# Kernel tuning notes

Measured on AMD Instinct MI355X. Metric: run time of the kernel, lower is better.

The kernel has to match this reference:

```python
import jax, jax.numpy as jnp
import numpy as np

B, N, M, R, W, H, NIN, OUT = 32, 1024, 64, 4, 1, 512, 256, 256
RM = 1 + 2 * W  # read modes: backward(W), content(1), forward(W)
SIZES = [W*M, W*M, R, W, W, R*RM, W*M, W, R*M, R]
OFFS = np.cumsum([0] + SIZES)
P = int(OFFS[-1])
EPS = 1e-8


def setup_inputs():
    key = jax.random.key(0)
    ks = jax.random.split(key, 20)
    norm = lambda w: w / jnp.sum(w, axis=-1, keepdims=True)
    return {
        'X': jax.random.normal(ks[0], (B, NIN), jnp.float32),
        'backward_embeddings': jax.random.normal(ks[1], (B, H), jnp.float32),
        'memory': jax.random.normal(ks[2], (B, N, M), jnp.float32) * 0.1,
        'prev_read': jax.random.normal(ks[3], (B, R, M), jnp.float32) * 0.01,
        'h0': jax.random.normal(ks[4], (B, H), jnp.float32) * 0.1,
        'c0': jax.random.normal(ks[5], (B, H), jnp.float32) * 0.1,
        'read_w_prev': norm(jax.random.uniform(ks[6], (B, R, N), jnp.float32)),
        'write_w_prev': norm(jax.random.uniform(ks[7], (B, W, N), jnp.float32)),
        'usage_prev': jax.random.uniform(ks[8], (B, W, N), jnp.float32) * 0.5,
        'prec_prev': norm(jax.random.uniform(ks[9], (B, W, N), jnp.float32)),
        'links_prev': jnp.zeros((B, W, N, N), jnp.float32),
        'lstm_Wx': jax.random.normal(ks[10], (NIN + R * M, 4 * H), jnp.float32) * 0.02,
        'lstm_Wh': jax.random.normal(ks[11], (H, 4 * H), jnp.float32) * 0.02,
        'lstm_b': jnp.zeros((4 * H,), jnp.float32),
        'para_W': jax.random.normal(ks[12], (2 * H, P), jnp.float32) * 0.02,
        'para_b': jax.random.normal(ks[13], (P,), jnp.float32) * 0.01,
        'ln_g': jnp.ones((P,), jnp.float32),
        'ln_b': jnp.zeros((P,), jnp.float32),
        'proc_W': jax.random.normal(ks[14], (2 * H + R * M, OUT), jnp.float32) * 0.02,
        'proc_b': jnp.zeros((OUT,), jnp.float32),
    }


def _content(keys, beta, mem):
    # cosine-similarity content addressing: keys [B,h,M], beta [B,h], mem [B,N,M] -> [B,h,N]
    kn = keys / (jnp.linalg.norm(keys, axis=-1, keepdims=True) + EPS)
    mn = mem / (jnp.linalg.norm(mem, axis=-1, keepdims=True) + EPS)
    sim = jnp.einsum('bhm,bnm->bhn', kn, mn)
    return jax.nn.softmax(beta[..., None] * sim, axis=-1)


def _layernorm(x, g, b):
    mu = jnp.mean(x, axis=-1, keepdims=True)
    var = jnp.var(x, axis=-1, keepdims=True)
    return (x - mu) / jnp.sqrt(var + 1e-5) * g + b


def reference(X, backward_embeddings, memory, prev_read, h0, c0,
              read_w_prev, write_w_prev, usage_prev, prec_prev, links_prev,
              lstm_Wx, lstm_Wh, lstm_b, para_W, para_b, ln_g, ln_b, proc_W, proc_b):
    # ---- controller (single LSTM step) ----
    inp = jnp.concatenate([X, prev_read.reshape(B, R * M)], axis=1)
    gates = inp @ lstm_Wx + h0 @ lstm_Wh + lstm_b
    i, f, g, o = jnp.split(gates, 4, axis=1)
    c = jax.nn.sigmoid(f) * c0 + jax.nn.sigmoid(i) * jnp.tanh(g)
    h = jax.nn.sigmoid(o) * jnp.tanh(c)  # c_output [B,H]

    # ---- param_operations ----
    pvec = _layernorm(jnp.concatenate([h, backward_embeddings], axis=1) @ para_W + para_b, ln_g, ln_b)
    sl = lambda k: pvec[:, OFFS[k]:OFFS[k + 1]]
    write_vectors = sl(0).reshape(B, W, M)
    erase_vectors = jax.nn.sigmoid(sl(1)).reshape(B, W, M)
    free_gate = jax.nn.sigmoid(sl(2))                      # [B,R]
    alloc_gate = jax.nn.sigmoid(sl(3))                     # [B,W]
    write_gate = jax.nn.sigmoid(sl(4))                     # [B,W]
    read_mode = jax.nn.softmax(sl(5).reshape(B, R, RM), axis=2)
    write_keys = sl(6).reshape(B, W, M)
    write_strengths = 1.0 + jax.nn.softplus(sl(7))         # [B,W]
    read_keys = sl(8).reshape(B, R, M)
    read_strengths = 1.0 + jax.nn.softplus(sl(9))          # [B,R]

    # ---- usage + allocation ----
    psi = jnp.prod(1.0 - free_gate[:, :, None] * read_w_prev, axis=1)          # [B,N]
    usage = (usage_prev + write_w_prev - usage_prev * write_w_prev) * psi[:, None, :]  # [B,W,N]
    order = jnp.argsort(usage, axis=-1)
    u_sorted = jnp.take_along_axis(usage, order, axis=-1)
    vals = (1.0 - u_sorted) * jnp.cumprod(u_sorted, axis=-1)  # inclusive cumprod (as in source)
    inv = jnp.argsort(order, axis=-1)
    alloc = jnp.take_along_axis(vals, inv, axis=-1)           # [B,W,N]

    # ---- write weights ----
    wc = _content(write_keys, write_strengths, memory)        # [B,W,N]
    ww = write_gate[..., None] * (alloc_gate[..., None] * alloc + (1.0 - alloc_gate[..., None]) * wc)

    # ---- memory write (sequential over write heads) ----
    mem = memory
    for wi in range(W):
        w = ww[:, wi]                                         # [B,N]
        mem = mem * (1.0 - w[:, :, None] * erase_vectors[:, wi, None, :]) \
              + w[:, :, None] * write_vectors[:, wi, None, :]

    # ---- temporal links ----
    eye = jnp.eye(N, dtype=mem.dtype)
    new_links, new_prec = [], []
    for wi in range(W):
        w = ww[:, wi]
        p = prec_prev[:, wi]
        L = links_prev[:, wi]
        Lnew = (1.0 - w[:, :, None] - w[:, None, :]) * L + w[:, :, None] * p[:, None, :]
        Lnew = Lnew * (1.0 - eye)                             # zero diagonal
        new_links.append(Lnew)
        new_prec.append((1.0 - jnp.sum(w, axis=1, keepdims=True)) * p + w)
    links = jnp.stack(new_links, axis=1)                      # [B,W,N,N]

    # ---- read weights: backward(W) | content | forward(W) ----
    rc = _content(read_keys, read_strengths, mem)             # [B,R,N]
    fwd = jnp.einsum('bwij,brj->bwri', links, read_w_prev)    # L @ w_prev
    bwd = jnp.einsum('bwji,brj->bwri', links, read_w_prev)    # L^T @ w_prev
    rw = read_mode[:, :, W][..., None] * rc
    for wi in range(W):
        rw = rw + read_mode[:, :, wi][..., None] * bwd[:, wi] \
                + read_mode[:, :, W + 1 + wi][..., None] * fwd[:, wi]

    # ---- reads + output projection ----
    reads = jnp.einsum('brn,bnm->brm', rw, mem)               # [B,R,M]
    out = jnp.concatenate([h, backward_embeddings, reads.reshape(B, R * M)], axis=1) @ proc_W + proc_b
    return out
```

## Files before the change

kernel.cpp:

```cpp
#include <hip/hip_runtime.h>
#include <math.h>

#define Bb 32
#define Nn 1024
#define Mm 64
#define Rr 4
#define Hh 512
#define NINq 256
#define Pp 471
#define EPSN 1e-8f

__device__ __forceinline__ float sigm(float x){ return 1.0f/(1.0f+expf(-x)); }

__global__ __launch_bounds__(256) void k_gates(
    const float* __restrict__ X, const float* __restrict__ pr,
    const float* __restrict__ h0, const float* __restrict__ Wx,
    const float* __restrict__ Wh, float* __restrict__ gpart)
{
  __shared__ float lin[32][64];
  int tid = threadIdx.x;
  int col = blockIdx.x*64 + (tid & 63);
  int bg  = tid >> 6;
  int k0  = blockIdx.y*64;
#pragma unroll
  for (int q=0;q<8;q++){
    int idx = tid + 256*q;
    int bb = idx >> 6, kk = idx & 63;
    int k = k0 + kk;
    float v;
    if (k < 256)      v = X [bb*NINq + k];
    else if (k < 512) v = pr[bb*(Rr*Mm) + (k-256)];
    else              v = h0[bb*Hh + (k-512)];
    lin[bb][kk] = v;
  }
  __syncthreads();
  const float* Wr = (k0 < 512) ? (Wx + (size_t)k0*2048)
                               : (Wh + (size_t)(k0-512)*2048);
  float acc[8];
#pragma unroll
  for (int i=0;i<8;i++) acc[i]=0.f;
#pragma unroll 8
  for (int kk=0; kk<64; ++kk){
    float wv = Wr[(size_t)kk*2048 + col];
#pragma unroll
    for (int bb=0; bb<8; ++bb) acc[bb] += wv * lin[bg*8+bb][kk];
  }
  float* gp = gpart + (size_t)blockIdx.y*65536;
#pragma unroll
  for (int bb=0; bb<8; ++bb)
    gp[(bg*8+bb)*2048 + col] = acc[bb];
}

__global__ void k_lstm_ep(const float* __restrict__ gpart, const float* __restrict__ lb,
                          const float* __restrict__ c0, const float* __restrict__ emb,
                          float* __restrict__ hcat, float* __restrict__ ocat)
{
  int idx = blockIdx.x*blockDim.x + threadIdx.x;
  if (idx >= Bb*Hh) return;
  int b = idx >> 9, j = idx & 511;
  float gi = lb[j], gf = lb[j+512], gg = lb[j+1024], go = lb[j+1536];
  for (int c=0;c<16;++c){
    const float* gp = gpart + (size_t)c*65536 + b*2048;
    gi += gp[j]; gf += gp[j+512]; gg += gp[j+1024]; go += gp[j+1536];
  }
  float c = sigm(gf)*c0[idx] + sigm(gi)*tanhf(gg);
  float h = sigm(go)*tanhf(c);
  float e = emb[idx];
  hcat[b*1024 + j]       = h;
  hcat[b*1024 + 512 + j] = e;
  ocat[b*1280 + j]       = h;
  ocat[b*1280 + 512 + j] = e;
  if (j < 256) ocat[b*1280 + 1024 + j] = 0.f;
}

__global__ __launch_bounds__(256) void k_para(
    const float* __restrict__ hcat, const float* __restrict__ Wp,
    float* __restrict__ ppart)
{
  __shared__ float lin[32][64];
  int tid = threadIdx.x;
  int col = blockIdx.x*64 + (tid & 63);
  int bg  = tid >> 6;
  int k0  = blockIdx.y*64;
#pragma unroll
  for (int q=0;q<8;q++){
    int idx = tid + 256*q;
    int bb = idx >> 6, kk = idx & 63;
    lin[bb][kk] = hcat[bb*1024 + k0 + kk];
  }
  __syncthreads();
  int colc = (col < Pp) ? col : (Pp-1);
  const float* Wr = Wp + (size_t)k0*Pp;
  float acc[8];
#pragma unroll
  for (int i=0;i<8;i++) acc[i]=0.f;
#pragma unroll 8
  for (int kk=0; kk<64; ++kk){
    float wv = Wr[(size_t)kk*Pp + colc];
#pragma unroll
    for (int bb=0; bb<8; ++bb) acc[bb] += wv * lin[bg*8+bb][kk];
  }
  if (col < Pp) {
    float* pp = ppart + (size_t)blockIdx.y*16384;
#pragma unroll
    for (int bb=0; bb<8; ++bb)
      pp[(bg*8+bb)*512 + col] = acc[bb];
  }
}

__global__ __launch_bounds__(1024) void k_lnalloc(
    const float* __restrict__ ppart, const float* __restrict__ bp,
    const float* __restrict__ ln_g, const float* __restrict__ ln_b,
    const float* __restrict__ rwp, const float* __restrict__ wwp,
    const float* __restrict__ up,
    float* __restrict__ pvec, float* __restrict__ alloc)
{
  __shared__ float red[8];
  __shared__ float fg[4];
  __shared__ unsigned long long sk[1024];
  __shared__ float wsums[16];
  int b = blockIdx.x, tid = threadIdx.x;
  int lane = tid & 63, wv = tid >> 6;
  float acc = 0.f, d = 0.f;
  if (tid < 512) {
    if (tid < Pp) {
      acc = bp[tid];
#pragma unroll
      for (int c=0;c<16;++c) acc += ppart[(size_t)c*16384 + b*512 + tid];
    }
    float s = acc;
    for (int o=32;o;o>>=1) s += __shfl_xor(s,o,64);
    if (lane==0) red[wv] = s;
  }
  __syncthreads();
  if (tid < 8){ float xx = red[tid]; for (int o=4;o;o>>=1) xx += __shfl_xor(xx,o,64); if (!tid) red[0]=xx; }
  __syncthreads();
  float mu = red[0] / (float)Pp;
  __syncthreads();
  if (tid < 512) {
    d = (tid < Pp) ? (acc - mu) : 0.f;
    float s2 = d*d;
    for (int o=32;o;o>>=1) s2 += __shfl_xor(s2,o,64);
    if (lane==0) red[wv] = s2;
  }
  __syncthreads();
  if (tid < 8){ float xx = red[tid]; for (int o=4;o;o>>=1) xx += __shfl_xor(xx,o,64); if (!tid) red[0]=xx; }
  __syncthreads();
  float var = red[0] / (float)Pp;
  if (tid < Pp) {
    float y = d / sqrtf(var + 1e-5f) * ln_g[tid] + ln_b[tid];
    pvec[b*512 + tid] = y;
    if (tid >= 128 && tid < 132) fg[tid-128] = sigm(y);
  }
  __syncthreads();
  float psi = 1.f;
#pragma unroll
  for (int r=0;r<4;r++) psi *= 1.f - fg[r]*rwp[b*(Rr*Nn) + r*Nn + tid];
  float u = up[b*Nn+tid], w = wwp[b*Nn+tid];
  float usage = (u + w - u*w)*psi;
  unsigned long long key = ((unsigned long long)__float_as_uint(usage) << 32) | (unsigned)tid;
  for (int k=2; k<=1024; k<<=1) {
    for (int j=k>>1; j>0; j>>=1) {
      bool lower = (tid & j) == 0;
      bool asc   = (tid & k) == 0;
      unsigned long long pk;
      if (j >= 64) {
        sk[tid] = key; __syncthreads();
        pk = sk[tid ^ j];
        __syncthreads();
      } else {
        pk = __shfl_xor(key, j, 64);
      }
      key = ((key < pk) == (lower == asc)) ? key : pk;
    }
  }
  float us = __uint_as_float((unsigned)(key >> 32));
  int order = (int)(key & 1023u);
  float v = us;
#pragma unroll
  for (int dd=1; dd<64; dd<<=1) {
    float p = __shfl_up(v, dd, 64);
    if (lane >= dd) v *= p;
  }
  if (lane == 63) wsums[wv] = v;
  __syncthreads();
  if (wv == 0) {
    float t = (lane < 16) ? wsums[lane] : 1.f;
#pragma unroll
    for (int dd=1; dd<16; dd<<=1) {
      float p = __shfl_up(t, dd, 64);
      if (lane >= dd) t *= p;
    }
    if (lane < 16) wsums[lane] = t;
  }
  __syncthreads();
  float prefix = (wv > 0) ? wsums[wv-1] : 1.f;
  alloc[b*Nn + order] = (1.f - us) * (v * prefix);
}

__global__ __launch_bounds__(256) void k_simw(
    const float* __restrict__ pvec, const float* __restrict__ mem,
    float* __restrict__ simw)
{
  __shared__ float kdir[64];
  __shared__ float sc[1];
  int b = blockIdx.y, tid = threadIdx.x;
  int wv = tid>>6, lane = tid&63;
  const float* pv = pvec + b*512;
  if (wv == 0) {
    float v = pv[146 + lane];
    float s = v*v;
    for (int o=32;o;o>>=1) s += __shfl_xor(s,o,64);
    kdir[lane] = v / (sqrtf(s) + EPSN);
    if (lane == 0) sc[0] = 1.f + log1pf(expf(pv[210]));
  }
  __syncthreads();
  float beta = sc[0];
  for (int t=0;t<16;++t){
    int n = blockIdx.x*64 + wv*16 + t;
    float v = mem[(b*Nn+n)*Mm + lane];
    float d = v*kdir[lane], s2 = v*v;
    for (int o=32;o;o>>=1){ d += __shfl_xor(d,o,64); s2 += __shfl_xor(s2,o,64); }
    if (lane == 0) simw[b*Nn+n] = beta * d / (sqrtf(s2) + EPSN);
  }
}

__global__ __launch_bounds__(1024) void k_ww2(
    const float* __restrict__ pvec, const float* __restrict__ simw,
    const float* __restrict__ alloc, const float* __restrict__ prec,
    const float* __restrict__ rwp, float* __restrict__ wwb, float* __restrict__ spsw)
{
  __shared__ float red[16];
  __shared__ float red8[16][8];
  __shared__ float scal[2];
  int b = blockIdx.x, tid = threadIdx.x;
  int wv = tid >> 6, lane = tid & 63;
  const float* pv = pvec + b*512;
  if (tid == 0) { scal[0] = sigm(pv[132]); scal[1] = sigm(pv[133]); }
  float v = simw[b*Nn + tid];
  float m_ = v;
  for (int o=32;o;o>>=1) m_ = fmaxf(m_, __shfl_xor(m_,o,64));
  if (lane==0) red[wv] = m_;
  __syncthreads();
  if (tid < 16){ float x = red[tid]; for (int o=8;o;o>>=1) x = fmaxf(x,__shfl_xor(x,o,64)); if (!tid) red[0]=x; }
  __syncthreads();
  float gmax = red[0];
  __syncthreads();
  float e = expf(v - gmax);
  float ss = e;
  for (int o=32;o;o>>=1) ss += __shfl_xor(ss,o,64);
  if (lane==0) red[wv] = ss;
  __syncthreads();
  if (tid < 16){ float x = red[tid]; for (int o=8;o;o>>=1) x += __shfl_xor(x,o,64); if (!tid) red[0]=x; }
  __syncthreads();
  float wcn = e / red[0];
  float ag = scal[0], wg = scal[1];
  float an = alloc[b*Nn + tid];
  float wwn = wg * (ag*an + (1.f-ag)*wcn);
  wwb[b*Nn + tid] = wwn;
  float p = prec[b*Nn + tid];
#pragma unroll
  for (int r=0;r<4;r++){
    float a = rwp[b*(Rr*Nn) + r*Nn + tid];
    float x1 = p*a, x2 = wwn*a;
    for (int o=32;o;o>>=1){ x1 += __shfl_xor(x1,o,64); x2 += __shfl_xor(x2,o,64); }
    if (lane==0){ red8[wv][r] = x1; red8[wv][4+r] = x2; }
  }
  __syncthreads();
  if (tid < 8) {
    float s = 0.f;
    for (int w2=0; w2<16; ++w2) s += red8[w2][tid];
    spsw[b*8 + tid] = s;
  }
}

__global__ __launch_bounds__(256) void k_memupd(
    const float* __restrict__ pvec, const float* __restrict__ mem,
    const float* __restrict__ wwb, float* __restrict__ memn, float* __restrict__ simr)
{
  __shared__ float ev[64], wvv[64];
  __shared__ float kdir[4][64];
  __shared__ float beta[4];
  int b = blockIdx.y, tid = threadIdx.x;
  int wv = tid>>6, lane = tid&63;
  const float* pv = pvec + b*512;
  {
    float kv = pv[211 + wv*64 + lane];
    float s = kv*kv;
    for (int o=32;o;o>>=1) s += __shfl_xor(s,o,64);
    kdir[wv][lane] = kv/(sqrtf(s)+EPSN);
    if (lane==0) beta[wv] = 1.f + log1pf(expf(pv[467+wv]));
  }
  if (tid < 64) { wvv[tid] = pv[tid]; ev[tid] = sigm(pv[64+tid]); }
  __syncthreads();
  for (int t=0;t<16;++t){
    int n = blockIdx.x*64 + wv*16 + t;
    float wwn = wwb[b*Nn + n];
    float v = mem[(b*Nn+n)*Mm + lane];
    float nv = v*(1.f - wwn*ev[lane]) + wwn*wvv[lane];
    memn[(b*Nn+n)*Mm + lane] = nv;
    float s2 = nv*nv;
    float d0 = nv*kdir[0][lane], d1 = nv*kdir[1][lane];
    float d2 = nv*kdir[2][lane], d3 = nv*kdir[3][lane];
    for (int o=32;o;o>>=1){
      s2 += __shfl_xor(s2,o,64);
      d0 += __shfl_xor(d0,o,64); d1 += __shfl_xor(d1,o,64);
      d2 += __shfl_xor(d2,o,64); d3 += __shfl_xor(d3,o,64);
    }
    if (lane==0){
      float inv = 1.f/(sqrtf(s2)+EPSN);
      simr[(b*4+0)*Nn+n] = beta[0]*d0*inv;
      simr[(b*4+1)*Nn+n] = beta[1]*d1*inv;
      simr[(b*4+2)*Nn+n] = beta[2]*d2*inv;
      simr[(b*4+3)*Nn+n] = beta[3]*d3*inv;
    }
  }
}

__global__ __launch_bounds__(256) void k_links(
    const float* __restrict__ links, const float* __restrict__ rwp,
    const float* __restrict__ wwb,
    float* __restrict__ S1p, float* __restrict__ S2p,
    float* __restrict__ T1p, float* __restrict__ T2p,
    float* __restrict__ diag)
{
  __shared__ float tile[64][65];
  __shared__ float ai[4][64], wai[4][64], aj[4][64], waj[4][64];
  int b = blockIdx.y;
  int stripe = blockIdx.x >> 1, half = blockIdx.x & 1;
  int i0 = stripe*64, jbase = half*512;
  int tid = threadIdx.x;
  {
    int r = tid>>6, ii = tid&63;
    float a = rwp[b*(Rr*Nn) + r*Nn + i0+ii];
    ai[r][ii]  = a;
    wai[r][ii] = a * wwb[b*Nn + i0+ii];
  }
  float s1a[4]={0,0,0,0}, s2a[4]={0,0,0,0};
  const float* Lb = links + (size_t)b*Nn*Nn;
  const int lrow = tid>>4, c4 = tid&15;
  float4 pv[4];
#pragma unroll
  for (int q=0;q<4;q++)
    pv[q] = *reinterpret_cast<const float4*>(&Lb[(size_t)(i0+lrow+16*q)*Nn + jbase + c4*4]);
  const int dt = (half == (stripe>>3)) ? (stripe&7) : -1;
  for (int t=0; t<8; ++t) {
    int j0 = jbase + t*64;
    __syncthreads();
#pragma unroll
    for (int q=0;q<4;q++){
      int row = lrow + 16*q;
      float4 v = pv[q];
      tile[row][c4*4+0]=v.x; tile[row][c4*4+1]=v.y;
      tile[row][c4*4+2]=v.z; tile[row][c4*4+3]=v.w;
    }
    {
      int r = tid>>6, jj = tid&63;
      float a = rwp[b*(Rr*Nn) + r*Nn + j0+jj];
      aj[r][jj]  = a;
      waj[r][jj] = a * wwb[b*Nn + j0+jj];
    }
    __syncthreads();
    if (t < 7) {
      int j0n = j0 + 64;
#pragma unroll
      for (int q=0;q<4;q++)
        pv[q] = *reinterpret_cast<const float4*>(&Lb[(size_t)(i0+lrow+16*q)*Nn + j0n + c4*4]);
    }
    if (t == dt && tid < 64) diag[b*Nn + i0 + tid] = tile[tid][tid];
    {
      int ii = tid>>2, c = tid&3;
      float p1[4]={0,0,0,0}, p2[4]={0,0,0,0};
      for (int k=0;k<16;k++){
        int jj = c*16+k;
        float v = tile[ii][jj];
#pragma unroll
        for (int r=0;r<4;r++){ p1[r] += v*aj[r][jj]; p2[r] += v*waj[r][jj]; }
      }
#pragma unroll
      for (int r=0;r<4;r++){
        p1[r] += __shfl_xor(p1[r],1,64); p1[r] += __shfl_xor(p1[r],2,64);
        p2[r] += __shfl_xor(p2[r],1,64); p2[r] += __shfl_xor(p2[r],2,64);
      }
      if (c==0){
#pragma unroll
        for (int r=0;r<4;r++){ s1a[r] += p1[r]; s2a[r] += p2[r]; }
      }
    }
    {
      int jj = tid>>2, q = tid&3;
      float p1[4]={0,0,0,0}, p2[4]={0,0,0,0};
      for (int k=0;k<16;k++){
        int ii = q*16+k;
        float v = tile[ii][jj];
#pragma unroll
        for (int r=0;r<4;r++){ p1[r] += v*ai[r][ii]; p2[r] += v*wai[r][ii]; }
      }
#pragma unroll
      for (int r=0;r<4;r++){
        p1[r] += __shfl_xor(p1[r],1,64); p1[r] += __shfl_xor(p1[r],2,64);
        p2[r] += __shfl_xor(p2[r],1,64); p2[r] += __shfl_xor(p2[r],2,64);
      }
      if (q==0){
#pragma unroll
        for (int r=0;r<4;r++){
          size_t o = (size_t)(((b*4+r)*16 + stripe))*Nn + j0 + jj;
          T1p[o] = p1[r];
          T2p[o] = p2[r];
        }
      }
    }
  }
  if ((tid&3)==0){
    int ii = tid>>2;
#pragma unroll
    for (int r=0;r<4;r++){
      size_t o = (size_t)(((half*Bb + b)*4 + r))*Nn + i0 + ii;
      S1p[o] = s1a[r];
      S2p[o] = s2a[r];
    }
  }
}

__global__ __launch_bounds__(1024) void k_rsoft(
    const float* __restrict__ pvec, const float* __restrict__ rwp,
    const float* __restrict__ prec, const float* __restrict__ wwb,
    const float* __restrict__ T1p, const float* __restrict__ T2p,
    const float* __restrict__ S1p, const float* __restrict__ S2p,
    const float* __restrict__ spsw, const float* __restrict__ diag,
    float* __restrict__ simr)
{
  __shared__ float red[16];
  __shared__ float rm3[3];
  int b = blockIdx.x, r = blockIdx.y, tid = threadIdx.x;
  int wv = tid>>6, lane = tid&63;
  const float* pv = pvec + b*512;
  if (tid == 0) {
    float x0 = pv[134+r*3], x1 = pv[134+r*3+1], x2 = pv[134+r*3+2];
    float mx = fmaxf(x0, fmaxf(x1,x2));
    float e0 = expf(x0-mx), e1 = expf(x1-mx), e2 = expf(x2-mx);
    float s = e0+e1+e2;
    rm3[0]=e0/s; rm3[1]=e1/s; rm3[2]=e2/s;
  }
  float v = simr[(b*4+r)*Nn + tid];
  float m_ = v;
  for (int o=32;o;o>>=1) m_ = fmaxf(m_, __shfl_xor(m_,o,64));
  if (lane==0) red[wv]=m_;
  __syncthreads();
  if (tid<16){ float x=red[tid]; for(int o=8;o;o>>=1) x=fmaxf(x,__shfl_xor(x,o,64)); if(!tid) red[0]=x; }
  __syncthreads();
  float gmax = red[0];
  __syncthreads();
  float e = expf(v-gmax);
  float s = e;
  for (int o=32;o;o>>=1) s += __shfl_xor(s,o,64);
  if (lane==0) red[wv]=s;
  __syncthreads();
  if (tid<16){ float x=red[tid]; for(int o=8;o;o>>=1) x+=__shfl_xor(x,o,64); if(!tid) red[0]=x; }
  __syncthreads();
  float rc = e/red[0];
  float s1v = S1p[(size_t)((0*Bb+b)*4+r)*Nn + tid] + S1p[(size_t)((1*Bb+b)*4+r)*Nn + tid];
  float s2v = S2p[(size_t)((0*Bb+b)*4+r)*Nn + tid] + S2p[(size_t)((1*Bb+b)*4+r)*Nn + tid];
  float t1v = 0.f, t2v = 0.f;
#pragma unroll
  for (int st=0; st<16; ++st){
    size_t o = (size_t)((b*4+r)*16 + st)*Nn + tid;
    t1v += T1p[o];
    t2v += T2p[o];
  }
  float w_n = wwb[b*Nn + tid];
  float p_n = prec[b*Nn + tid];
  float a = rwp[b*(Rr*Nn)+r*Nn+tid];
  float Lii = diag[b*Nn + tid];
  float Spr = spsw[b*8+r], Swr = spsw[b*8+4+r];
  float fwd = (1.f-w_n)*(s1v - Lii*a) - (s2v - Lii*w_n*a) + w_n*(Spr - p_n*a);
  float bwd = (1.f-w_n)*(t1v - Lii*a) - (t2v - w_n*Lii*a) + p_n*(Swr - w_n*a);
  simr[(b*4+r)*Nn + tid] = rm3[1]*rc + rm3[0]*bwd + rm3[2]*fwd;
}

__global__ __launch_bounds__(256) void k_rgemv(
    const float* __restrict__ simr, const float* __restrict__ memn,
    const float* __restrict__ bo, float* __restrict__ ocat, float* __restrict__ out)
{
  int b = blockIdx.y, ch = blockIdx.x, tid = threadIdx.x;
  if (ch == 0) out[b*256 + tid] = bo[tid];
  int r = tid>>6, m = tid&63;
  float acc = 0.f;
#pragma unroll 8
  for (int t=0;t<64;++t){
    int n = ch*64 + t;
    acc += simr[(b*4+r)*Nn + n] * memn[(b*Nn+n)*Mm + m];
  }
  atomicAdd(&ocat[b*1280 + 1024 + r*64 + m], acc);
}

__global__ __launch_bounds__(256) void k_gout(
    const float* __restrict__ ocat, const float* __restrict__ Wo,
    float* __restrict__ out)
{
  __shared__ float lin[32][64];
  int tid = threadIdx.x;
  int col = blockIdx.x*64 + (tid & 63);
  int bg  = tid >> 6;
  int k0  = blockIdx.y*64;
#pragma unroll
  for (int q=0;q<8;q++){
    int idx = tid + 256*q;
    int bb = idx >> 6, kk = idx & 63;
    lin[bb][kk] = ocat[bb*1280 + k0 + kk];
  }
  __syncthreads();
  const float* Wr = Wo + (size_t)k0*256;
  float acc[8];
#pragma unroll
  for (int i=0;i<8;i++) acc[i]=0.f;
#pragma unroll 8
  for (int kk=0; kk<64; ++kk){
    float wv = Wr[(size_t)kk*256 + col];
#pragma unroll
    for (int bb=0; bb<8; ++bb) acc[bb] += wv * lin[bg*8+bb][kk];
  }
#pragma unroll
  for (int bb=0; bb<8; ++bb)
    atomicAdd(&out[(size_t)(bg*8+bb)*256 + col], acc[bb]);
}

extern "C" void kernel_launch(void* const* d_in, const int* in_sizes, int n_in,
                              void* d_out, int out_size, void* d_ws, size_t ws_size,
                              hipStream_t stream)
{
  (void)in_sizes; (void)n_in; (void)out_size; (void)ws_size;
  const float* X    = (const float*)d_in[0];
  const float* emb  = (const float*)d_in[1];
  const float* mem  = (const float*)d_in[2];
  const float* prvr = (const float*)d_in[3];
  const float* h0   = (const float*)d_in[4];
  const float* c0   = (const float*)d_in[5];
  const float* rwp  = (const float*)d_in[6];
  const float* wwp  = (const float*)d_in[7];
  const float* up   = (const float*)d_in[8];
  const float* prec = (const float*)d_in[9];
  const float* links= (const float*)d_in[10];
  const float* Wx   = (const float*)d_in[11];
  const float* Wh   = (const float*)d_in[12];
  const float* lb   = (const float*)d_in[13];
  const float* Wp   = (const float*)d_in[14];
  const float* bp   = (const float*)d_in[15];
  const float* lng  = (const float*)d_in[16];
  const float* lnb  = (const float*)d_in[17];
  const float* Wo   = (const float*)d_in[18];
  const float* bo   = (const float*)d_in[19];
  float* out = (float*)d_out;
  float* ws  = (float*)d_ws;

  float* memn  = ws;
  float* T1p   = memn  + 2097152;
  float* T2p   = T1p   + 2097152;
  float* S1p   = T2p   + 2097152;
  float* S2p   = S1p   + 262144;
  float* gpart = S2p   + 262144;
  float* ppart = gpart + 1048576;
  float* pvec  = ppart + 262144;
  float* alloc = pvec  + 16384;
  float* wwb   = alloc + 32768;
  float* ocat  = wwb   + 32768;
  float* spsw  = ocat  + 40960;
  float* simr  = spsw  + 256;
  float* diag  = simr  + 131072;
  float* hcat  = diag  + 32768;

  k_gates  <<<dim3(32,16),  dim3(256),  0, stream>>>(X, prvr, h0, Wx, Wh, gpart);
  k_lstm_ep<<<dim3(64),     dim3(256),  0, stream>>>(gpart, lb, c0, emb, hcat, ocat);
  k_para   <<<dim3(8,16),   dim3(256),  0, stream>>>(hcat, Wp, ppart);
  k_lnalloc<<<dim3(32),     dim3(1024), 0, stream>>>(ppart, bp, lng, lnb, rwp, wwp, up, pvec, alloc);
  k_simw   <<<dim3(16,32),  dim3(256),  0, stream>>>(pvec, mem, simr);
  k_ww2    <<<dim3(32),     dim3(1024), 0, stream>>>(pvec, simr, alloc, prec, rwp, wwb, spsw);
  k_memupd <<<dim3(16,32),  dim3(256),  0, stream>>>(pvec, mem, wwb, memn, simr);
  k_links  <<<dim3(32,32),  dim3(256),  0, stream>>>(links, rwp, wwb, S1p, S2p, T1p, T2p, diag);
  k_rsoft  <<<dim3(32,4),   dim3(1024), 0, stream>>>(pvec, rwp, prec, wwb, T1p, T2p, S1p, S2p, spsw, diag, simr);
  k_rgemv  <<<dim3(16,32),  dim3(256),  0, stream>>>(simr, memn, bo, ocat, out);
  k_gout   <<<dim3(4,20),   dim3(256),  0, stream>>>(ocat, Wo, out);
}
```

Baseline: 134.9 us.

## Fuse write-addressing, links/memory update, and read path into fewer kernels

Folds the write-content similarity and the write-weight softmax into the layernorm/allocation kernel, so the allocation vector stays in shared memory. The memory update and read-content similarity now run as extra blocks of the links kernel, and the read softmax, read weighting and read GEMV are merged into one per-batch kernel that no longer needs atomics. Eleven launches become seven and several global round trips go away. In exchange, the write-similarity and read-GEMV work now runs on only 32 blocks, each doing per-thread row loads, so parallelism on those parts drops.

```diff
diff --git a/kernel.cpp b/kernel.cpp
--- a/kernel.cpp
+++ b/kernel.cpp
@@ -70,7 +70,6 @@
   hcat[b*1024 + 512 + j] = e;
   ocat[b*1280 + j]       = h;
   ocat[b*1280 + 512 + j] = e;
-  if (j < 256) ocat[b*1280 + 1024 + j] = 0.f;
 }
 
 __global__ __launch_bounds__(256) void k_para(
@@ -108,17 +107,23 @@
   }
 }
 
-__global__ __launch_bounds__(1024) void k_lnalloc(
+__global__ __launch_bounds__(1024) void k_waddr(
     const float* __restrict__ ppart, const float* __restrict__ bp,
     const float* __restrict__ ln_g, const float* __restrict__ ln_b,
     const float* __restrict__ rwp, const float* __restrict__ wwp,
-    const float* __restrict__ up,
-    float* __restrict__ pvec, float* __restrict__ alloc)
-{
-  __shared__ float red[8];
+    const float* __restrict__ up, const float* __restrict__ mem,
+    const float* __restrict__ prec,
+    float* __restrict__ pvec, float* __restrict__ wwb, float* __restrict__ spsw)
+{
+  __shared__ float red[16];
+  __shared__ float pvs[512];
   __shared__ float fg[4];
+  __shared__ float kdir[64];
+  __shared__ float scal[4];
   __shared__ unsigned long long sk[1024];
   __shared__ float wsums[16];
+  __shared__ float af[1024];
+  __shared__ float red8[16][8];
   int b = blockIdx.x, tid = threadIdx.x;
   int lane = tid & 63, wv = tid >> 6;
   float acc = 0.f, d = 0.f;
@@ -150,7 +155,20 @@
   if (tid < Pp) {
     float y = d / sqrtf(var + 1e-5f) * ln_g[tid] + ln_b[tid];
     pvec[b*512 + tid] = y;
-    if (tid >= 128 && tid < 132) fg[tid-128] = sigm(y);
+    pvs[tid] = y;
+  }
+  __syncthreads();
+  if (tid < 4) fg[tid] = sigm(pvs[128+tid]);
+  if (wv == 0) {
+    float v = pvs[146 + lane];
+    float s = v*v;
+    for (int o=32;o;o>>=1) s += __shfl_xor(s,o,64);
+    kdir[lane] = v / (sqrtf(s) + EPSN);
+  }
+  if (tid == 0) {
+    scal[0] = sigm(pvs[132]);
+    scal[1] = sigm(pvs[133]);
+    scal[2] = 1.f + log1pf(expf(pvs[210]));
   }
   __syncthreads();
   float psi = 1.f;
@@ -195,50 +213,18 @@
   }
   __syncthreads();
   float prefix = (wv > 0) ? wsums[wv-1] : 1.f;
-  alloc[b*Nn + order] = (1.f - us) * (v * prefix);
-}
-
-__global__ __launch_bounds__(256) void k_simw(
-    const float* __restrict__ pvec, const float* __restrict__ mem,
-    float* __restrict__ simw)
-{
-  __shared__ float kdir[64];
-  __shared__ float sc[1];
-  int b = blockIdx.y, tid = threadIdx.x;
-  int wv = tid>>6, lane = tid&63;
-  const float* pv = pvec + b*512;
-  if (wv == 0) {
-    float v = pv[146 + lane];
-    float s = v*v;
-    for (int o=32;o;o>>=1) s += __shfl_xor(s,o,64);
-    kdir[lane] = v / (sqrtf(s) + EPSN);
-    if (lane == 0) sc[0] = 1.f + log1pf(expf(pv[210]));
-  }
-  __syncthreads();
-  float beta = sc[0];
-  for (int t=0;t<16;++t){
-    int n = blockIdx.x*64 + wv*16 + t;
-    float v = mem[(b*Nn+n)*Mm + lane];
-    float d = v*kdir[lane], s2 = v*v;
-    for (int o=32;o;o>>=1){ d += __shfl_xor(d,o,64); s2 += __shfl_xor(s2,o,64); }
-    if (lane == 0) simw[b*Nn+n] = beta * d / (sqrtf(s2) + EPSN);
-  }
-}
-
-__global__ __launch_bounds__(1024) void k_ww2(
-    const float* __restrict__ pvec, const float* __restrict__ simw,
-    const float* __restrict__ alloc, const float* __restrict__ prec,
-    const float* __restrict__ rwp, float* __restrict__ wwb, float* __restrict__ spsw)
-{
-  __shared__ float red[16];
-  __shared__ float red8[16][8];
-  __shared__ float scal[2];
-  int b = blockIdx.x, tid = threadIdx.x;
-  int wv = tid >> 6, lane = tid & 63;
-  const float* pv = pvec + b*512;
-  if (tid == 0) { scal[0] = sigm(pv[132]); scal[1] = sigm(pv[133]); }
-  float v = simw[b*Nn + tid];
-  float m_ = v;
+  af[order] = (1.f - us) * (v * prefix);
+  float beta = scal[2];
+  float dot = 0.f, s2 = 0.f;
+  const float* mrow = mem + (size_t)(b*Nn + tid)*Mm;
+#pragma unroll
+  for (int j=0;j<16;j++){
+    float4 mv = *reinterpret_cast<const float4*>(&mrow[j*4]);
+    dot += mv.x*kdir[j*4] + mv.y*kdir[j*4+1] + mv.z*kdir[j*4+2] + mv.w*kdir[j*4+3];
+    s2  += mv.x*mv.x + mv.y*mv.y + mv.z*mv.z + mv.w*mv.w;
+  }
+  float sim = beta * dot / (sqrtf(s2) + EPSN);
+  float m_ = sim;
   for (int o=32;o;o>>=1) m_ = fmaxf(m_, __shfl_xor(m_,o,64));
   if (lane==0) red[wv] = m_;
   __syncthreads();
@@ -246,7 +232,7 @@
   __syncthreads();
   float gmax = red[0];
   __syncthreads();
-  float e = expf(v - gmax);
+  float e = expf(sim - gmax);
   float ss = e;
   for (int o=32;o;o>>=1) ss += __shfl_xor(ss,o,64);
   if (lane==0) red[wv] = ss;
@@ -255,8 +241,7 @@
   __syncthreads();
   float wcn = e / red[0];
   float ag = scal[0], wg = scal[1];
-  float an = alloc[b*Nn + tid];
-  float wwn = wg * (ag*an + (1.f-ag)*wcn);
+  float wwn = wg * (ag*af[tid] + (1.f-ag)*wcn);
   wwb[b*Nn + tid] = wwn;
   float p = prec[b*Nn + tid];
 #pragma unroll
@@ -274,62 +259,60 @@
   }
 }
 
-__global__ __launch_bounds__(256) void k_memupd(
-    const float* __restrict__ pvec, const float* __restrict__ mem,
-    const float* __restrict__ wwb, float* __restrict__ memn, float* __restrict__ simr)
-{
-  __shared__ float ev[64], wvv[64];
-  __shared__ float kdir[4][64];
-  __shared__ float beta[4];
-  int b = blockIdx.y, tid = threadIdx.x;
-  int wv = tid>>6, lane = tid&63;
-  const float* pv = pvec + b*512;
-  {
-    float kv = pv[211 + wv*64 + lane];
-    float s = kv*kv;
-    for (int o=32;o;o>>=1) s += __shfl_xor(s,o,64);
-    kdir[wv][lane] = kv/(sqrtf(s)+EPSN);
-    if (lane==0) beta[wv] = 1.f + log1pf(expf(pv[467+wv]));
-  }
-  if (tid < 64) { wvv[tid] = pv[tid]; ev[tid] = sigm(pv[64+tid]); }
-  __syncthreads();
-  for (int t=0;t<16;++t){
-    int n = blockIdx.x*64 + wv*16 + t;
-    float wwn = wwb[b*Nn + n];
-    float v = mem[(b*Nn+n)*Mm + lane];
-    float nv = v*(1.f - wwn*ev[lane]) + wwn*wvv[lane];
-    memn[(b*Nn+n)*Mm + lane] = nv;
-    float s2 = nv*nv;
-    float d0 = nv*kdir[0][lane], d1 = nv*kdir[1][lane];
-    float d2 = nv*kdir[2][lane], d3 = nv*kdir[3][lane];
-    for (int o=32;o;o>>=1){
-      s2 += __shfl_xor(s2,o,64);
-      d0 += __shfl_xor(d0,o,64); d1 += __shfl_xor(d1,o,64);
-      d2 += __shfl_xor(d2,o,64); d3 += __shfl_xor(d3,o,64);
-    }
-    if (lane==0){
-      float inv = 1.f/(sqrtf(s2)+EPSN);
-      simr[(b*4+0)*Nn+n] = beta[0]*d0*inv;
-      simr[(b*4+1)*Nn+n] = beta[1]*d1*inv;
-      simr[(b*4+2)*Nn+n] = beta[2]*d2*inv;
-      simr[(b*4+3)*Nn+n] = beta[3]*d3*inv;
-    }
-  }
-}
-
-__global__ __launch_bounds__(256) void k_links(
+__global__ __launch_bounds__(256) void k_linksmem(
     const float* __restrict__ links, const float* __restrict__ rwp,
-    const float* __restrict__ wwb,
+    const float* __restrict__ wwb, const float* __restrict__ pvec,
+    const float* __restrict__ mem,
     float* __restrict__ S1p, float* __restrict__ S2p,
     float* __restrict__ T1p, float* __restrict__ T2p,
-    float* __restrict__ diag)
-{
+    float* __restrict__ diag, float* __restrict__ memn, float* __restrict__ simr)
+{
+  int b = blockIdx.y;
+  int tid = threadIdx.x;
+  if (blockIdx.x >= 32) {
+    __shared__ float ev[64], wvv[64];
+    __shared__ float kdir4[4][64];
+    __shared__ float beta4[4];
+    int stripe = blockIdx.x - 32;
+    int wv = tid>>6, lane = tid&63;
+    const float* pv = pvec + b*512;
+    {
+      float kv = pv[211 + wv*64 + lane];
+      float s = kv*kv;
+      for (int o=32;o;o>>=1) s += __shfl_xor(s,o,64);
+      kdir4[wv][lane] = kv/(sqrtf(s)+EPSN);
+      if (lane==0) beta4[wv] = 1.f + log1pf(expf(pv[467+wv]));
+    }
+    if (tid < 64) { wvv[tid] = pv[tid]; ev[tid] = sigm(pv[64+tid]); }
+    __syncthreads();
+    for (int t=0;t<16;++t){
+      int n = stripe*64 + wv*16 + t;
+      float wwn = wwb[b*Nn + n];
+      float v = mem[(b*Nn+n)*Mm + lane];
+      float nv = v*(1.f - wwn*ev[lane]) + wwn*wvv[lane];
+      memn[(b*Nn+n)*Mm + lane] = nv;
+      float s2 = nv*nv;
+      float d0 = nv*kdir4[0][lane], d1 = nv*kdir4[1][lane];
+      float d2 = nv*kdir4[2][lane], d3 = nv*kdir4[3][lane];
+      for (int o=32;o;o>>=1){
+        s2 += __shfl_xor(s2,o,64);
+        d0 += __shfl_xor(d0,o,64); d1 += __shfl_xor(d1,o,64);
+        d2 += __shfl_xor(d2,o,64); d3 += __shfl_xor(d3,o,64);
+      }
+      if (lane==0){
+        float inv = 1.f/(sqrtf(s2)+EPSN);
+        simr[(b*4+0)*Nn+n] = beta4[0]*d0*inv;
+        simr[(b*4+1)*Nn+n] = beta4[1]*d1*inv;
+        simr[(b*4+2)*Nn+n] = beta4[2]*d2*inv;
+        simr[(b*4+3)*Nn+n] = beta4[3]*d3*inv;
+      }
+    }
+    return;
+  }
   __shared__ float tile[64][65];
   __shared__ float ai[4][64], wai[4][64], aj[4][64], waj[4][64];
-  int b = blockIdx.y;
   int stripe = blockIdx.x >> 1, half = blockIdx.x & 1;
   int i0 = stripe*64, jbase = half*512;
-  int tid = threadIdx.x;
   {
     int r = tid>>6, ii = tid&63;
     float a = rwp[b*(Rr*Nn) + r*Nn + i0+ii];
@@ -422,76 +405,83 @@
   }
 }
 
-__global__ __launch_bounds__(1024) void k_rsoft(
+__global__ __launch_bounds__(1024) void k_rread(
     const float* __restrict__ pvec, const float* __restrict__ rwp,
     const float* __restrict__ prec, const float* __restrict__ wwb,
     const float* __restrict__ T1p, const float* __restrict__ T2p,
     const float* __restrict__ S1p, const float* __restrict__ S2p,
     const float* __restrict__ spsw, const float* __restrict__ diag,
-    float* __restrict__ simr)
-{
+    const float* __restrict__ simr, const float* __restrict__ memn,
+    const float* __restrict__ bo, float* __restrict__ ocat, float* __restrict__ out)
+{
+  __shared__ float rwl[4][1024];
   __shared__ float red[16];
-  __shared__ float rm3[3];
-  int b = blockIdx.x, r = blockIdx.y, tid = threadIdx.x;
+  __shared__ float rm3s[4][3];
+  __shared__ float rp[16][4][64];
+  int b = blockIdx.x, tid = threadIdx.x;
   int wv = tid>>6, lane = tid&63;
   const float* pv = pvec + b*512;
-  if (tid == 0) {
-    float x0 = pv[134+r*3], x1 = pv[134+r*3+1], x2 = pv[134+r*3+2];
+  if (tid < 4) {
+    float x0 = pv[134+tid*3], x1 = pv[134+tid*3+1], x2 = pv[134+tid*3+2];
     float mx = fmaxf(x0, fmaxf(x1,x2));
     float e0 = expf(x0-mx), e1 = expf(x1-mx), e2 = expf(x2-mx);
     float s = e0+e1+e2;
-    rm3[0]=e0/s; rm3[1]=e1/s; rm3[2]=e2/s;
-  }
-  float v = simr[(b*4+r)*Nn + tid];
-  float m_ = v;
-  for (int o=32;o;o>>=1) m_ = fmaxf(m_, __shfl_xor(m_,o,64));
-  if (lane==0) red[wv]=m_;
-  __syncthreads();
-  if (tid<16){ float x=red[tid]; for(int o=8;o;o>>=1) x=fmaxf(x,__shfl_xor(x,o,64)); if(!tid) red[0]=x; }
-  __syncthreads();
-  float gmax = red[0];
-  __syncthreads();
-  float e = expf(v-gmax);
-  float s = e;
-  for (int o=32;o;o>>=1) s += __shfl_xor(s,o,64);
-  if (lane==0) red[wv]=s;
-  __syncthreads();
-  if (tid<16){ float x=red[tid]; for(int o=8;o;o>>=1) x+=__shfl_xor(x,o,64); if(!tid) red[0]=x; }
-  __syncthreads();
-  float rc = e/red[0];
-  float s1v = S1p[(size_t)((0*Bb+b)*4+r)*Nn + tid] + S1p[(size_t)((1*Bb+b)*4+r)*Nn + tid];
-  float s2v = S2p[(size_t)((0*Bb+b)*4+r)*Nn + tid] + S2p[(size_t)((1*Bb+b)*4+r)*Nn + tid];
-  float t1v = 0.f, t2v = 0.f;
-#pragma unroll
-  for (int st=0; st<16; ++st){
-    size_t o = (size_t)((b*4+r)*16 + st)*Nn + tid;
-    t1v += T1p[o];
-    t2v += T2p[o];
+    rm3s[tid][0]=e0/s; rm3s[tid][1]=e1/s; rm3s[tid][2]=e2/s;
   }
   float w_n = wwb[b*Nn + tid];
   float p_n = prec[b*Nn + tid];
-  float a = rwp[b*(Rr*Nn)+r*Nn+tid];
   float Lii = diag[b*Nn + tid];
-  float Spr = spsw[b*8+r], Swr = spsw[b*8+4+r];
-  float fwd = (1.f-w_n)*(s1v - Lii*a) - (s2v - Lii*w_n*a) + w_n*(Spr - p_n*a);
-  float bwd = (1.f-w_n)*(t1v - Lii*a) - (t2v - w_n*Lii*a) + p_n*(Swr - w_n*a);
-  simr[(b*4+r)*Nn + tid] = rm3[1]*rc + rm3[0]*bwd + rm3[2]*fwd;
-}
-
-__global__ __launch_bounds__(256) void k_rgemv(
-    const float* __restrict__ simr, const float* __restrict__ memn,
-    const float* __restrict__ bo, float* __restrict__ ocat, float* __restrict__ out)
-{
-  int b = blockIdx.y, ch = blockIdx.x, tid = threadIdx.x;
-  if (ch == 0) out[b*256 + tid] = bo[tid];
-  int r = tid>>6, m = tid&63;
-  float acc = 0.f;
-#pragma unroll 8
+  __syncthreads();
+  for (int r=0;r<4;++r){
+    float v = simr[(b*4+r)*Nn + tid];
+    float m_ = v;
+    for (int o=32;o;o>>=1) m_ = fmaxf(m_, __shfl_xor(m_,o,64));
+    if (lane==0) red[wv]=m_;
+    __syncthreads();
+    if (tid<16){ float x=red[tid]; for(int o=8;o;o>>=1) x=fmaxf(x,__shfl_xor(x,o,64)); if(!tid) red[0]=x; }
+    __syncthreads();
+    float gmax = red[0];
+    __syncthreads();
+    float e = expf(v-gmax);
+    float s = e;
+    for (int o=32;o;o>>=1) s += __shfl_xor(s,o,64);
+    if (lane==0) red[wv]=s;
+    __syncthreads();
+    if (tid<16){ float x=red[tid]; for(int o=8;o;o>>=1) x+=__shfl_xor(x,o,64); if(!tid) red[0]=x; }
+    __syncthreads();
+    float rc = e/red[0];
+    float s1v = S1p[(size_t)((0*Bb+b)*4+r)*Nn + tid] + S1p[(size_t)((1*Bb+b)*4+r)*Nn + tid];
+    float s2v = S2p[(size_t)((0*Bb+b)*4+r)*Nn + tid] + S2p[(size_t)((1*Bb+b)*4+r)*Nn + tid];
+    float t1v = 0.f, t2v = 0.f;
+#pragma unroll
+    for (int st=0; st<16; ++st){
+      size_t o = (size_t)((b*4+r)*16 + st)*Nn + tid;
+      t1v += T1p[o];
+      t2v += T2p[o];
+    }
+    float a = rwp[b*(Rr*Nn)+r*Nn+tid];
+    float Spr = spsw[b*8+r], Swr = spsw[b*8+4+r];
+    float fwd = (1.f-w_n)*(s1v - Lii*a) - (s2v - Lii*w_n*a) + w_n*(Spr - p_n*a);
+    float bwd = (1.f-w_n)*(t1v - Lii*a) - (t2v - w_n*Lii*a) + p_n*(Swr - w_n*a);
+    rwl[r][tid] = rm3s[r][1]*rc + rm3s[r][0]*bwd + rm3s[r][2]*fwd;
+    __syncthreads();
+  }
+  float a0=0.f, a1=0.f, a2=0.f, a3=0.f;
   for (int t=0;t<64;++t){
-    int n = ch*64 + t;
-    acc += simr[(b*4+r)*Nn + n] * memn[(b*Nn+n)*Mm + m];
-  }
-  atomicAdd(&ocat[b*1280 + 1024 + r*64 + m], acc);
+    int n = wv*64 + t;
+    float v = memn[(size_t)(b*Nn+n)*Mm + lane];
+    a0 += rwl[0][n]*v; a1 += rwl[1][n]*v; a2 += rwl[2][n]*v; a3 += rwl[3][n]*v;
+  }
+  rp[wv][0][lane]=a0; rp[wv][1][lane]=a1; rp[wv][2][lane]=a2; rp[wv][3][lane]=a3;
+  __syncthreads();
+  if (tid < 256) {
+    int r = tid>>6, m = tid&63;
+    float s = 0.f;
+#pragma unroll
+    for (int w2=0;w2<16;++w2) s += rp[w2][r][m];
+    ocat[b*1280 + 1024 + r*64 + m] = s;
+    out[b*256 + tid] = bo[tid];
+  }
 }
 
 __global__ __launch_bounds__(256) void k_gout(
@@ -561,23 +551,22 @@
   float* gpart = S2p   + 262144;
   float* ppart = gpart + 1048576;
   float* pvec  = ppart + 262144;
-  float* alloc = pvec  + 16384;
-  float* wwb   = alloc + 32768;
+  float* wwb   = pvec  + 16384;
   float* ocat  = wwb   + 32768;
   float* spsw  = ocat  + 40960;
   float* simr  = spsw  + 256;
   float* diag  = simr  + 131072;
   float* hcat  = diag  + 32768;
 
-  k_gates  <<<dim3(32,16),  dim3(256),  0, stream>>>(X, prvr, h0, Wx, Wh, gpart);
-  k_lstm_ep<<<dim3(64),     dim3(256),  0, stream>>>(gpart, lb, c0, emb, hcat, ocat);
-  k_para   <<<dim3(8,16),   dim3(256),  0, stream>>>(hcat, Wp, ppart);
-  k_lnalloc<<<dim3(32),     dim3(1024), 0, stream>>>(ppart, bp, lng, lnb, rwp, wwp, up, pvec, alloc);
-  k_simw   <<<dim3(16,32),  dim3(256),  0, stream>>>(pvec, mem, simr);
-  k_ww2    <<<dim3(32),     dim3(1024), 0, stream>>>(pvec, simr, alloc, prec, rwp, wwb, spsw);
-  k_memupd <<<dim3(16,32),  dim3(256),  0, stream>>>(pvec, mem, wwb, memn, simr);
-  k_links  <<<dim3(32,32),  dim3(256),  0, stream>>>(links, rwp, wwb, S1p, S2p, T1p, T2p, diag);
-  k_rsoft  <<<dim3(32,4),   dim3(1024), 0, stream>>>(pvec, rwp, prec, wwb, T1p, T2p, S1p, S2p, spsw, diag, simr);
-  k_rgemv  <<<dim3(16,32),  dim3(256),  0, stream>>>(simr, memn, bo, ocat, out);
-  k_gout   <<<dim3(4,20),   dim3(256),  0, stream>>>(ocat, Wo, out);
-}
+  k_gates   <<<dim3(32,16), dim3(256),  0, stream>>>(X, prvr, h0, Wx, Wh, gpart);
+  k_lstm_ep <<<dim3(64),    dim3(256),  0, stream>>>(gpart, lb, c0, emb, hcat, ocat);
+  k_para    <<<dim3(8,16),  dim3(256),  0, stream>>>(hcat, Wp, ppart);
+  k_waddr   <<<dim3(32),    dim3(1024), 0, stream>>>(ppart, bp, lng, lnb, rwp, wwp, up,
+                                                     mem, prec, pvec, wwb, spsw);
+  k_linksmem<<<dim3(48,32), dim3(256),  0, stream>>>(links, rwp, wwb, pvec, mem,
+                                                     S1p, S2p, T1p, T2p, diag, memn, simr);
+  k_rread   <<<dim3(32),    dim3(1024), 0, stream>>>(pvec, rwp, prec, wwb, T1p, T2p,
+                                                     S1p, S2p, spsw, diag, simr, memn,
+                                                     bo, ocat, out);
+  k_gout    <<<dim3(4,20),  dim3(256),  0, stream>>>(ocat, Wo, out);
+}
```

Measured after the change: 133.0 us. Within noise of the previous version (-1.5%).
